# Kernel tuning notes

Hardware: AMD Instinct MI355X
Metric: run time of the kernel (lower is better)

Reference implementation:

```python
import jax, jax.numpy as jnp
import numpy as np

WS = 10
NUM_HEADS = 12
DIM = 384


def setup_inputs() -> dict:
    key = jax.random.key(0)
    k1, k2, k3 = jax.random.split(key, 3)
    B, t, H, W, C = 2, 4, 44, 44, DIM
    x = jax.random.normal(k1, (B * t, H * W, C), dtype=jnp.float32)
    qkv_w = jax.random.normal(k2, (3 * C, C), dtype=jnp.float32) * 0.02
    proj_w = jax.random.normal(k3, (C, C), dtype=jnp.float32) * 0.02
    proj_b = jnp.zeros((C,), dtype=jnp.float32)
    return {"x": x, "qkv_w": qkv_w, "proj_w": proj_w, "proj_b": proj_b,
            "t": t, "H": H, "W": W}


def reference(x, qkv_w, proj_w, proj_b, t, H, W):
    ws, nh = WS, NUM_HEADS
    BT, N, C = x.shape
    B = BT // t
    hd = C // nh
    scale = hd ** (-0.5)

    ax = x.reshape(B, t, H, W, C)
    pad_r = (ws - W % ws) % ws
    pad_b = (ws - H % ws) % ws
    if pad_r > 0 or pad_b > 0:
        ax = jnp.pad(ax, ((0, 0), (0, 0), (0, pad_b), (0, pad_r), (0, 0)))
    hg, wg = (H + ws - 1) // ws, (W + ws - 1) // ws
    # partition into windows: each window holds t*ws*ws tokens
    ax = ax.reshape(B, t, hg, ws, wg, ws, C)
    ax = ax.transpose(0, 2, 4, 1, 3, 5, 6).reshape(B, hg * wg, t * ws * ws, C)

    qkv = ax @ qkv_w.T  # (B, nw, n, 3C)
    qkv = qkv.reshape(B, hg * wg, t * ws * ws, 3, nh, hd)
    qkv = qkv.transpose(3, 0, 1, 4, 2, 5)  # (3, B, nw, nh, n, hd)
    q, k, v = qkv[0], qkv[1], qkv[2]

    attn = jnp.einsum('bwhnd,bwhmd->bwhnm', q, k) * scale
    attn = jax.nn.softmax(attn, axis=-1)
    out = jnp.einsum('bwhnm,bwhmd->bwhnd', attn, v)  # (B, nw, nh, n, hd)
    out = out.transpose(0, 1, 3, 2, 4).reshape(B, hg * wg, t * ws * ws, C)

    # reverse window partition
    out = out.reshape(B, hg, wg, t, ws, ws, C)
    out = out.transpose(0, 3, 1, 4, 2, 5, 6).reshape(B, t, hg * ws, wg * ws, C)
    out = out[:, :, :H, :W, :]
    out = out.reshape(B, t * H * W, C)
    out = out @ proj_w.T + proj_b
    return out.reshape(-1, N, C)
```

## Files before the change

kernel.cpp:

```cpp
#include <hip/hip_runtime.h>
#include <cstddef>

typedef __attribute__((ext_vector_type(8))) short bf16x8;
typedef __attribute__((ext_vector_type(4))) float f32x4;
typedef __attribute__((ext_vector_type(16))) float f32x16;
typedef unsigned short ushort_t;

namespace {
constexpr int Tt = 4, Hh = 44, Ww = 44, Cc = 384, NH = 12, HD = 32;
constexpr int NWIN = 25, NT = 400, NPOS = Hh * Ww;
constexpr int NTOK = 2 * Tt * NPOS;
constexpr float SCALE = 0.17677669529663687f;
constexpr float LOG2E = 1.4426950408889634f;
constexpr size_t XN  = (size_t)NTOK * Cc;
constexpr size_t WN  = (size_t)3 * Cc * Cc;
constexpr size_t PWN = (size_t)Cc * Cc;
constexpr size_t QKVN = (size_t)NTOK * 3 * Cc;
}

__device__ __forceinline__ ushort_t f2bf(float f) {
  unsigned u = __builtin_bit_cast(unsigned, f);
  u += 0x7fffu + ((u >> 16) & 1u);
  return (ushort_t)(u >> 16);
}

__device__ __forceinline__ unsigned cvt_pk_bf16(float a, float b) {
  unsigned r;
  asm volatile("v_cvt_pk_bf16_f32 %0, %1, %2" : "=v"(r) : "v"(a), "v"(b));
  return r;
}

__device__ __forceinline__ bf16x8 bf8zero() {
  bf16x8 v;
  v[0] = 0; v[1] = 0; v[2] = 0; v[3] = 0;
  v[4] = 0; v[5] = 0; v[6] = 0; v[7] = 0;
  return v;
}

__device__ __forceinline__ void gload16(const void* g, void* l) {
  __builtin_amdgcn_global_load_lds(
      (const __attribute__((address_space(1))) unsigned int*)g,
      (__attribute__((address_space(3))) unsigned int*)l, 16, 0, 0);
}

__device__ __forceinline__ bool win_tok(int kk, int b, int hi5, int wi5,
                                        int& tok) {
  const int tt = kk / 100, rem = kk - tt * 100;
  const int hh = rem / 10, ww2 = rem - hh * 10;
  const int h = hi5 * 10 + hh, w = wi5 * 10 + ww2;
  tok = (b * Tt + tt) * NPOS + h * Ww + w;
  return (kk < NT) && (h < Hh) && (w < Ww);
}

__global__ __launch_bounds__(256) void conv_all(
    const float* __restrict__ x, const float* __restrict__ w1,
    const float* __restrict__ w2, ushort_t* __restrict__ xo,
    ushort_t* __restrict__ w1o, ushort_t* __restrict__ w2o) {
  constexpr int XN8 = (int)(XN / 8), WN8 = (int)(WN / 8), PN8 = (int)(PWN / 8);
  int i = blockIdx.x * 256 + threadIdx.x;
  if (i >= XN8 + WN8 + PN8) return;
  const float* s;
  ushort_t* d;
  int j;
  if (i < XN8)            { s = x;  d = xo;  j = i; }
  else if (i < XN8 + WN8) { s = w1; d = w1o; j = i - XN8; }
  else                    { s = w2; d = w2o; j = i - XN8 - WN8; }
  const float4* s4 = (const float4*)s;
  float4 a = s4[2 * j], bq = s4[2 * j + 1];
  union { bf16x8 v; ushort_t u[8]; } o;
  o.u[0] = f2bf(a.x);  o.u[1] = f2bf(a.y);  o.u[2] = f2bf(a.z);  o.u[3] = f2bf(a.w);
  o.u[4] = f2bf(bq.x); o.u[5] = f2bf(bq.y); o.u[6] = f2bf(bq.z); o.u[7] = f2bf(bq.w);
  ((bf16x8*)d)[j] = o.v;
}

__global__ __launch_bounds__(256) void qkv_mfma(
    const ushort_t* __restrict__ xb, const ushort_t* __restrict__ wb,
    ushort_t* __restrict__ qkvb) {
  __shared__ __align__(16) unsigned char As[8192];
  __shared__ __align__(16) unsigned char Bs[8192];
  const int nt = blockIdx.x, mt = blockIdx.y;
  const int tid = threadIdx.x, lane = tid & 63, wid = tid >> 6;
  const int wm = wid >> 1, wn = wid & 1;
  const int g = lane >> 4, q = lane & 15;
  const int m0 = mt * 128, n0 = nt * 128;

  const unsigned char* xB = (const unsigned char*)xb;
  const unsigned char* wB = (const unsigned char*)wb;

  size_t aoff[2], boff[2];
  unsigned ldsoff[2];
#pragma unroll
  for (int p = 0; p < 2; ++p) {
    const int row = wid * 32 + p * 16 + (lane >> 2);
    const int gs = (lane & 3) ^ ((row >> 1) & 3);
    aoff[p] = (size_t)(m0 + row) * 768 + gs * 16;
    boff[p] = (size_t)(n0 + row) * 768 + gs * 16;
    ldsoff[p] = wid * 2048 + p * 1024;
  }

  f32x4 acc[4][4] = {};

  for (int kb = 0; kb < 12; ++kb) {
    if (kb) __syncthreads();
#pragma unroll
    for (int p = 0; p < 2; ++p) {
      gload16(xB + aoff[p] + kb * 64, As + ldsoff[p]);
      gload16(wB + boff[p] + kb * 64, Bs + ldsoff[p]);
    }
    __syncthreads();
    bf16x8 afr[4], bfr[4];
#pragma unroll
    for (int i = 0; i < 4; ++i) {
      const int ar = wm * 64 + i * 16 + q;
      afr[i] = *(const bf16x8*)(As + ar * 64 + ((g ^ ((ar >> 1) & 3)) << 4));
      const int br = wn * 64 + i * 16 + q;
      bfr[i] = *(const bf16x8*)(Bs + br * 64 + ((g ^ ((br >> 1) & 3)) << 4));
    }
#pragma unroll
    for (int i = 0; i < 4; ++i)
#pragma unroll
      for (int j = 0; j < 4; ++j)
        acc[i][j] = __builtin_amdgcn_mfma_f32_16x16x32_bf16(afr[i], bfr[j],
                                                            acc[i][j], 0, 0, 0);
  }

  const float QS = SCALE * LOG2E;
#pragma unroll
  for (int j = 0; j < 4; ++j) {
    const int col = n0 + wn * 64 + j * 16 + q;
    const float scl = (col < Cc) ? QS : 1.0f;
#pragma unroll
    for (int i = 0; i < 4; ++i) {
      const int rbase = m0 + wm * 64 + i * 16 + 4 * g;
#pragma unroll
      for (int r = 0; r < 4; ++r)
        qkvb[(size_t)(rbase + r) * 1152 + col] = f2bf(acc[i][j][r] * scl);
    }
  }
}

__global__ __launch_bounds__(512) void attn_mfma(
    const ushort_t* __restrict__ qkvb, ushort_t* __restrict__ aout) {
  __shared__ __align__(16) unsigned char Vt[32 * 896];

  const int blk = blockIdx.x;
  const int strip = blk & 1;
  const int wh = blk >> 1;
  const int head = wh % NH, bw = wh / NH;
  const int b = bw / NWIN, win = bw % NWIN, hi5 = win / 5, wi5 = win % 5;
  const int hoff = head * HD;

  const int tid = threadIdx.x, lane = tid & 63, wid = tid >> 6;

  for (int slot = tid; slot < 1664; slot += 512) {
    const int key = slot >> 2, dblk = (slot & 3) * 8;
    int tok;
    union { bf16x8 v; ushort_t u[8]; } t;
    if (win_tok(key, b, hi5, wi5, tok)) {
      t.v = *(const bf16x8*)(qkvb + (size_t)tok * 1152 + 768 + hoff + dblk);
    } else {
      t.v = bf8zero();
    }
    const int kc = key >> 3, klo = key & 7;
#pragma unroll
    for (int j = 0; j < 8; ++j) {
      const int d = dblk + j;
      const int f = (d & 7) ^ ((d >> 3) & 3);
      *(ushort_t*)(Vt + d * 896 + ((kc ^ f) << 4) + klo * 2) = t.u[j];
    }
  }
  __syncthreads();

  if (strip == 1 && wid >= 5) return;

  const int l31 = lane & 31, hi = lane >> 5;
  const int qrow = strip * 256 + wid * 32 + l31;
  int qtok;
  const bool qv = win_tok(qrow, b, hi5, wi5, qtok);
  const int qsrc = qv ? qtok : 0;

  const ushort_t* qp = qkvb + (size_t)qsrc * 1152 + hoff;
  const bf16x8 qf0 = *(const bf16x8*)(qp);
  const bf16x8 qf1 = *(const bf16x8*)(qp + 16);
  const bf16x8 qfa = *(const bf16x8*)(qp + hi * 8);
  const bf16x8 qfb = *(const bf16x8*)(qp + 16 + hi * 8);
  (void)qf0; (void)qf1;

  bf16x8 kf0, kf1;
  {
    int tok;
    if (win_tok(l31, b, hi5, wi5, tok)) {
      const ushort_t* kp = qkvb + (size_t)tok * 1152 + 384 + hoff;
      kf0 = *(const bf16x8*)(kp + hi * 8);
      kf1 = *(const bf16x8*)(kp + 16 + hi * 8);
    } else {
      kf0 = bf8zero();
      kf1 = bf8zero();
    }
  }

  const int fv = (l31 & 7) ^ ((l31 >> 3) & 3);
  const unsigned char* vrow = Vt + l31 * 896;

  f32x16 o = {};
  float mrun = -1e30f, lrun = 0.f;

  for (int c = 0; c < 13; ++c) {
    f32x16 s = {};
    s = __builtin_amdgcn_mfma_f32_32x32x16_bf16(kf0, qfa, s, 0, 0, 0);
    s = __builtin_amdgcn_mfma_f32_32x32x16_bf16(kf1, qfb, s, 0, 0, 0);

    if (c < 12) {
      int tok;
      if (win_tok((c + 1) * 32 + l31, b, hi5, wi5, tok)) {
        const ushort_t* kp = qkvb + (size_t)tok * 1152 + 384 + hoff;
        kf0 = *(const bf16x8*)(kp + hi * 8);
        kf1 = *(const bf16x8*)(kp + 16 + hi * 8);
      } else {
        kf0 = bf8zero();
        kf1 = bf8zero();
      }
    }

    if (c == 12) {
#pragma unroll
      for (int r = 8; r < 16; ++r) s[r] = -1e30f;
    }

    float m01 = fmaxf(s[0], s[1]),   m23 = fmaxf(s[2], s[3]);
    float m45 = fmaxf(s[4], s[5]),   m67 = fmaxf(s[6], s[7]);
    float m89 = fmaxf(s[8], s[9]),   mab = fmaxf(s[10], s[11]);
    float mcd = fmaxf(s[12], s[13]), mef = fmaxf(s[14], s[15]);
    float mc = fmaxf(fmaxf(fmaxf(m01, m23), fmaxf(m45, m67)),
                     fmaxf(fmaxf(m89, mab), fmaxf(mcd, mef)));
    mc = fmaxf(mc, __shfl_xor(mc, 32));
    const float mnew = fmaxf(mrun, mc);
    const float cf = __builtin_amdgcn_exp2f(mrun - mnew);
    mrun = mnew;

    float e[16];
#pragma unroll
    for (int r = 0; r < 16; ++r) e[r] = __builtin_amdgcn_exp2f(s[r] - mnew);
    float ps = ((e[0] + e[1]) + (e[2] + e[3])) + ((e[4] + e[5]) + (e[6] + e[7])) +
               (((e[8] + e[9]) + (e[10] + e[11])) +
                ((e[12] + e[13]) + (e[14] + e[15])));
    ps += __shfl_xor(ps, 32);
    lrun = lrun * cf + ps;
#pragma unroll
    for (int r = 0; r < 16; ++r) o[r] *= cf;

    unsigned w0 = cvt_pk_bf16(e[0], e[1]),   w1 = cvt_pk_bf16(e[2], e[3]);
    unsigned w2 = cvt_pk_bf16(e[4], e[5]),   w3 = cvt_pk_bf16(e[6], e[7]);
    unsigned w4 = cvt_pk_bf16(e[8], e[9]),   w5 = cvt_pk_bf16(e[10], e[11]);
    unsigned w6 = cvt_pk_bf16(e[12], e[13]), w7 = cvt_pk_bf16(e[14], e[15]);
    asm volatile("v_permlane32_swap_b32 %0, %1" : "+v"(w0), "+v"(w2));
    asm volatile("v_permlane32_swap_b32 %0, %1" : "+v"(w1), "+v"(w3));
    asm volatile("v_permlane32_swap_b32 %0, %1" : "+v"(w4), "+v"(w6));
    asm volatile("v_permlane32_swap_b32 %0, %1" : "+v"(w5), "+v"(w7));
    union { bf16x8 v; unsigned u[4]; } p0, p1;
    p0.u[0] = w0; p0.u[1] = w1; p0.u[2] = w2; p0.u[3] = w3;
    p1.u[0] = w4; p1.u[1] = w5; p1.u[2] = w6; p1.u[3] = w7;

    const bf16x8 vf0 = *(const bf16x8*)(vrow + (((4 * c + hi) ^ fv) << 4));
    const bf16x8 vf1 = *(const bf16x8*)(vrow + (((4 * c + 2 + hi) ^ fv) << 4));
    o = __builtin_amdgcn_mfma_f32_32x32x16_bf16(vf0, p0.v, o, 0, 0, 0);
    o = __builtin_amdgcn_mfma_f32_32x32x16_bf16(vf1, p1.v, o, 0, 0, 0);
  }

  if (qv) {
    ushort_t* dst = aout + (size_t)qtok * Cc + hoff;
    const float inv = 1.0f / lrun;
#pragma unroll
    for (int g4 = 0; g4 < 4; ++g4) {
      unsigned lo  = cvt_pk_bf16(o[4 * g4 + 0] * inv, o[4 * g4 + 1] * inv);
      unsigned hi2 = cvt_pk_bf16(o[4 * g4 + 2] * inv, o[4 * g4 + 3] * inv);
      uint2 st; st.x = lo; st.y = hi2;
      *(uint2*)(dst + 8 * g4 + 4 * hi) = st;
    }
  }
}

__global__ __launch_bounds__(256) void proj_mfma(
    const ushort_t* __restrict__ ab, const ushort_t* __restrict__ pw,
    const float* __restrict__ bias, float* __restrict__ out) {
  __shared__ __align__(16) unsigned char As[8192];
  __shared__ __align__(16) unsigned char Bs[8192];
  const int nt = blockIdx.x, mt = blockIdx.y;
  const int tid = threadIdx.x, lane = tid & 63, wid = tid >> 6;
  const int wm = wid >> 1, wn = wid & 1;
  const int g = lane >> 4, q = lane & 15;
  const int m0 = mt * 128, n0 = nt * 128;

  const unsigned char* aB = (const unsigned char*)ab;
  const unsigned char* wB = (const unsigned char*)pw;

  size_t aoff[2], boff[2];
  unsigned ldsoff[2];
#pragma unroll
  for (int p = 0; p < 2; ++p) {
    const int row = wid * 32 + p * 16 + (lane >> 2);
    const int gs = (lane & 3) ^ ((row >> 1) & 3);
    aoff[p] = (size_t)(m0 + row) * 768 + gs * 16;
    boff[p] = (size_t)(n0 + row) * 768 + gs * 16;
    ldsoff[p] = wid * 2048 + p * 1024;
  }

  f32x4 acc[4][4] = {};

  for (int kb = 0; kb < 12; ++kb) {
    if (kb) __syncthreads();
#pragma unroll
    for (int p = 0; p < 2; ++p) {
      gload16(aB + aoff[p] + kb * 64, As + ldsoff[p]);
      gload16(wB + boff[p] + kb * 64, Bs + ldsoff[p]);
    }
    __syncthreads();
    bf16x8 afr[4], bfr[4];
#pragma unroll
    for (int i = 0; i < 4; ++i) {
      const int ar = wm * 64 + i * 16 + q;
      afr[i] = *(const bf16x8*)(As + ar * 64 + ((g ^ ((ar >> 1) & 3)) << 4));
      const int br = wn * 64 + i * 16 + q;
      bfr[i] = *(const bf16x8*)(Bs + br * 64 + ((g ^ ((br >> 1) & 3)) << 4));
    }
#pragma unroll
    for (int i = 0; i < 4; ++i)
#pragma unroll
      for (int j = 0; j < 4; ++j)
        acc[i][j] = __builtin_amdgcn_mfma_f32_16x16x32_bf16(afr[i], bfr[j],
                                                            acc[i][j], 0, 0, 0);
  }

#pragma unroll
  for (int j = 0; j < 4; ++j) {
    const int col = n0 + wn * 64 + j * 16 + q;
    const float bj = bias[col];
#pragma unroll
    for (int i = 0; i < 4; ++i) {
      const int rbase = m0 + wm * 64 + i * 16 + 4 * g;
#pragma unroll
      for (int r = 0; r < 4; ++r)
        out[(size_t)(rbase + r) * Cc + col] = acc[i][j][r] + bj;
    }
  }
}

extern "C" void kernel_launch(void* const* d_in, const int* in_sizes, int n_in,
                              void* d_out, int out_size, void* d_ws,
                              size_t ws_size, hipStream_t stream) {
  const float* x      = (const float*)d_in[0];
  const float* qkv_w  = (const float*)d_in[1];
  const float* proj_w = (const float*)d_in[2];
  const float* proj_b = (const float*)d_in[3];

  ushort_t* xb    = (ushort_t*)d_ws;
  ushort_t* wb    = xb + XN;
  ushort_t* pwb   = wb + WN;
  ushort_t* qkvb  = pwb + PWN;
  ushort_t* attnb = qkvb + QKVN;

  constexpr int TOT8 = (int)((XN + WN + PWN) / 8);
  conv_all<<<(TOT8 + 255) / 256, 256, 0, stream>>>(x, qkv_w, proj_w, xb, wb, pwb);
  qkv_mfma<<<dim3(9, 121), 256, 0, stream>>>(xb, wb, qkvb);
  attn_mfma<<<1200, 512, 0, stream>>>(qkvb, attnb);
  proj_mfma<<<dim3(3, 121), 256, 0, stream>>>(attnb, pwb, proj_b, (float*)d_out);
}
```

Measured before the change: 100.00 us.

## Scatter QKV into window-major padded layout and drop online softmax max tracking

```diff
diff --git a/kernel.cpp b/kernel.cpp
--- a/kernel.cpp
+++ b/kernel.cpp
@@ -10,12 +10,13 @@
 constexpr int Tt = 4, Hh = 44, Ww = 44, Cc = 384, NH = 12, HD = 32;
 constexpr int NWIN = 25, NT = 400, NPOS = Hh * Ww;
 constexpr int NTOK = 2 * Tt * NPOS;
+constexpr int NWROW = 2 * NWIN * NT;
 constexpr float SCALE = 0.17677669529663687f;
 constexpr float LOG2E = 1.4426950408889634f;
 constexpr size_t XN  = (size_t)NTOK * Cc;
 constexpr size_t WN  = (size_t)3 * Cc * Cc;
 constexpr size_t PWN = (size_t)Cc * Cc;
-constexpr size_t QKVN = (size_t)NTOK * 3 * Cc;
+constexpr size_t QKVWN = (size_t)NWROW * 1152;
 }
 
 __device__ __forceinline__ ushort_t f2bf(float f) {
@@ -30,52 +31,56 @@
   return r;
 }
 
-__device__ __forceinline__ bf16x8 bf8zero() {
-  bf16x8 v;
-  v[0] = 0; v[1] = 0; v[2] = 0; v[3] = 0;
-  v[4] = 0; v[5] = 0; v[6] = 0; v[7] = 0;
-  return v;
-}
-
 __device__ __forceinline__ void gload16(const void* g, void* l) {
   __builtin_amdgcn_global_load_lds(
       (const __attribute__((address_space(1))) unsigned int*)g,
       (__attribute__((address_space(3))) unsigned int*)l, 16, 0, 0);
 }
 
-__device__ __forceinline__ bool win_tok(int kk, int b, int hi5, int wi5,
-                                        int& tok) {
-  const int tt = kk / 100, rem = kk - tt * 100;
-  const int hh = rem / 10, ww2 = rem - hh * 10;
-  const int h = hi5 * 10 + hh, w = wi5 * 10 + ww2;
-  tok = (b * Tt + tt) * NPOS + h * Ww + w;
-  return (kk < NT) && (h < Hh) && (w < Ww);
-}
-
 __global__ __launch_bounds__(256) void conv_all(
     const float* __restrict__ x, const float* __restrict__ w1,
     const float* __restrict__ w2, ushort_t* __restrict__ xo,
-    ushort_t* __restrict__ w1o, ushort_t* __restrict__ w2o) {
+    ushort_t* __restrict__ w1o, ushort_t* __restrict__ w2o,
+    ushort_t* __restrict__ qkvw) {
   constexpr int XN8 = (int)(XN / 8), WN8 = (int)(WN / 8), PN8 = (int)(PWN / 8);
-  int i = blockIdx.x * 256 + threadIdx.x;
-  if (i >= XN8 + WN8 + PN8) return;
-  const float* s;
-  ushort_t* d;
-  int j;
-  if (i < XN8)            { s = x;  d = xo;  j = i; }
-  else if (i < XN8 + WN8) { s = w1; d = w1o; j = i - XN8; }
-  else                    { s = w2; d = w2o; j = i - XN8 - WN8; }
-  const float4* s4 = (const float4*)s;
-  float4 a = s4[2 * j], bq = s4[2 * j + 1];
-  union { bf16x8 v; ushort_t u[8]; } o;
-  o.u[0] = f2bf(a.x);  o.u[1] = f2bf(a.y);  o.u[2] = f2bf(a.z);  o.u[3] = f2bf(a.w);
-  o.u[4] = f2bf(bq.x); o.u[5] = f2bf(bq.y); o.u[6] = f2bf(bq.z); o.u[7] = f2bf(bq.w);
-  ((bf16x8*)d)[j] = o.v;
+  constexpr int TOT8 = XN8 + WN8 + PN8;
+  constexpr int ZFN = NWROW * 9;
+  const int i = blockIdx.x * 256 + threadIdx.x;
+  if (i < TOT8) {
+    const float* s;
+    ushort_t* d;
+    int j;
+    if (i < XN8)            { s = x;  d = xo;  j = i; }
+    else if (i < XN8 + WN8) { s = w1; d = w1o; j = i - XN8; }
+    else                    { s = w2; d = w2o; j = i - XN8 - WN8; }
+    const float4* s4 = (const float4*)s;
+    float4 a = s4[2 * j], bq = s4[2 * j + 1];
+    union { bf16x8 v; ushort_t u[8]; } o;
+    o.u[0] = f2bf(a.x);  o.u[1] = f2bf(a.y);  o.u[2] = f2bf(a.z);  o.u[3] = f2bf(a.w);
+    o.u[4] = f2bf(bq.x); o.u[5] = f2bf(bq.y); o.u[6] = f2bf(bq.z); o.u[7] = f2bf(bq.w);
+    ((bf16x8*)d)[j] = o.v;
+  } else if (i < TOT8 + ZFN) {
+    const int j = i - TOT8;
+    const int row = j / 9, seg = j - row * 9;
+    const int bw = row / NT, kk = row - bw * NT;
+    const int win = bw % NWIN, hi5 = win / 5, wi5 = win % 5;
+    const int tt = kk / 100, rem = kk - tt * 100;
+    const int hh = rem / 10, ww2 = rem - hh * 10;
+    const bool invalid = (hi5 == 4 && hh >= 4) || (wi5 == 4 && ww2 >= 4);
+    (void)tt;
+    if (invalid) {
+      bf16x8* dst = (bf16x8*)(qkvw + (size_t)row * 1152 + seg * 128);
+      bf16x8 z;
+      z[0]=0;z[1]=0;z[2]=0;z[3]=0;z[4]=0;z[5]=0;z[6]=0;z[7]=0;
+#pragma unroll
+      for (int p = 0; p < 16; ++p) dst[p] = z;
+    }
+  }
 }
 
 __global__ __launch_bounds__(256) void qkv_mfma(
     const ushort_t* __restrict__ xb, const ushort_t* __restrict__ wb,
-    ushort_t* __restrict__ qkvb) {
+    ushort_t* __restrict__ qkvw) {
   __shared__ __align__(16) unsigned char As[8192];
   __shared__ __align__(16) unsigned char Bs[8192];
   const int nt = blockIdx.x, mt = blockIdx.y;
@@ -108,39 +113,47 @@
       gload16(wB + boff[p] + kb * 64, Bs + ldsoff[p]);
     }
     __syncthreads();
-    bf16x8 afr[4], bfr[4];
+    bf16x8 tfr[4], wfr[4];
 #pragma unroll
     for (int i = 0; i < 4; ++i) {
       const int ar = wm * 64 + i * 16 + q;
-      afr[i] = *(const bf16x8*)(As + ar * 64 + ((g ^ ((ar >> 1) & 3)) << 4));
+      tfr[i] = *(const bf16x8*)(As + ar * 64 + ((g ^ ((ar >> 1) & 3)) << 4));
       const int br = wn * 64 + i * 16 + q;
-      bfr[i] = *(const bf16x8*)(Bs + br * 64 + ((g ^ ((br >> 1) & 3)) << 4));
+      wfr[i] = *(const bf16x8*)(Bs + br * 64 + ((g ^ ((br >> 1) & 3)) << 4));
     }
 #pragma unroll
     for (int i = 0; i < 4; ++i)
 #pragma unroll
       for (int j = 0; j < 4; ++j)
-        acc[i][j] = __builtin_amdgcn_mfma_f32_16x16x32_bf16(afr[i], bfr[j],
+        acc[i][j] = __builtin_amdgcn_mfma_f32_16x16x32_bf16(wfr[i], tfr[j],
                                                             acc[i][j], 0, 0, 0);
   }
 
   const float QS = SCALE * LOG2E;
 #pragma unroll
   for (int j = 0; j < 4; ++j) {
-    const int col = n0 + wn * 64 + j * 16 + q;
-    const float scl = (col < Cc) ? QS : 1.0f;
+    const int t = m0 + wm * 64 + j * 16 + q;
+    const int bt = t / NPOS, pos = t - bt * NPOS;
+    const int h = pos / Ww, w = pos - h * Ww;
+    const int b = bt >> 2, tt = bt & 3;
+    const int hq = h / 10, wq = w / 10;
+    const int kk = tt * 100 + (h - hq * 10) * 10 + (w - wq * 10);
+    const int row = ((b * NWIN) + hq * 5 + wq) * NT + kk;
+    ushort_t* dst = qkvw + (size_t)row * 1152;
 #pragma unroll
     for (int i = 0; i < 4; ++i) {
-      const int rbase = m0 + wm * 64 + i * 16 + 4 * g;
-#pragma unroll
-      for (int r = 0; r < 4; ++r)
-        qkvb[(size_t)(rbase + r) * 1152 + col] = f2bf(acc[i][j][r] * scl);
+      const int col = n0 + wn * 64 + i * 16 + 4 * g;
+      const float scl = (col < Cc) ? QS : 1.0f;
+      uint2 st;
+      st.x = cvt_pk_bf16(acc[i][j][0] * scl, acc[i][j][1] * scl);
+      st.y = cvt_pk_bf16(acc[i][j][2] * scl, acc[i][j][3] * scl);
+      *(uint2*)(dst + col) = st;
     }
   }
 }
 
 __global__ __launch_bounds__(512) void attn_mfma(
-    const ushort_t* __restrict__ qkvb, ushort_t* __restrict__ aout) {
+    const ushort_t* __restrict__ qkvw, ushort_t* __restrict__ aout) {
   __shared__ __align__(16) unsigned char Vt[32 * 896];
 
   const int blk = blockIdx.x;
@@ -148,19 +161,15 @@
   const int wh = blk >> 1;
   const int head = wh % NH, bw = wh / NH;
   const int b = bw / NWIN, win = bw % NWIN, hi5 = win / 5, wi5 = win % 5;
-  const int hoff = head * HD;
 
   const int tid = threadIdx.x, lane = tid & 63, wid = tid >> 6;
+  const unsigned char* rowB = (const unsigned char*)(qkvw + (size_t)(bw * NT) * 1152);
 
   for (int slot = tid; slot < 1664; slot += 512) {
     const int key = slot >> 2, dblk = (slot & 3) * 8;
-    int tok;
+    const int kc8 = key < NT ? key : NT - 1;
     union { bf16x8 v; ushort_t u[8]; } t;
-    if (win_tok(key, b, hi5, wi5, tok)) {
-      t.v = *(const bf16x8*)(qkvb + (size_t)tok * 1152 + 768 + hoff + dblk);
-    } else {
-      t.v = bf8zero();
-    }
+    t.v = *(const bf16x8*)(rowB + (size_t)kc8 * 2304 + 1536 + head * 64 + dblk * 2);
     const int kc = key >> 3, klo = key & 7;
 #pragma unroll
     for (int j = 0; j < 8; ++j) {
@@ -175,35 +184,22 @@
 
   const int l31 = lane & 31, hi = lane >> 5;
   const int qrow = strip * 256 + wid * 32 + l31;
-  int qtok;
-  const bool qv = win_tok(qrow, b, hi5, wi5, qtok);
-  const int qsrc = qv ? qtok : 0;
-
-  const ushort_t* qp = qkvb + (size_t)qsrc * 1152 + hoff;
-  const bf16x8 qf0 = *(const bf16x8*)(qp);
-  const bf16x8 qf1 = *(const bf16x8*)(qp + 16);
-  const bf16x8 qfa = *(const bf16x8*)(qp + hi * 8);
-  const bf16x8 qfb = *(const bf16x8*)(qp + 16 + hi * 8);
-  (void)qf0; (void)qf1;
-
-  bf16x8 kf0, kf1;
-  {
-    int tok;
-    if (win_tok(l31, b, hi5, wi5, tok)) {
-      const ushort_t* kp = qkvb + (size_t)tok * 1152 + 384 + hoff;
-      kf0 = *(const bf16x8*)(kp + hi * 8);
-      kf1 = *(const bf16x8*)(kp + 16 + hi * 8);
-    } else {
-      kf0 = bf8zero();
-      kf1 = bf8zero();
-    }
-  }
+  const int qclamp = qrow < NT ? qrow : NT - 1;
+
+  const unsigned char* qp = rowB + (size_t)qclamp * 2304 + head * 64;
+  const bf16x8 qfa = *(const bf16x8*)(qp + hi * 16);
+  const bf16x8 qfb = *(const bf16x8*)(qp + 32 + hi * 16);
+
+  const unsigned char* kB = rowB + 768 + head * 64;
+  unsigned koff = (unsigned)l31 * 2304u;
+  bf16x8 kf0 = *(const bf16x8*)(kB + koff + hi * 16);
+  bf16x8 kf1 = *(const bf16x8*)(kB + koff + 32 + hi * 16);
 
   const int fv = (l31 & 7) ^ ((l31 >> 3) & 3);
   const unsigned char* vrow = Vt + l31 * 896;
 
   f32x16 o = {};
-  float mrun = -1e30f, lrun = 0.f;
+  float lpart = 0.f;
 
   for (int c = 0; c < 13; ++c) {
     f32x16 s = {};
@@ -211,15 +207,10 @@
     s = __builtin_amdgcn_mfma_f32_32x32x16_bf16(kf1, qfb, s, 0, 0, 0);
 
     if (c < 12) {
-      int tok;
-      if (win_tok((c + 1) * 32 + l31, b, hi5, wi5, tok)) {
-        const ushort_t* kp = qkvb + (size_t)tok * 1152 + 384 + hoff;
-        kf0 = *(const bf16x8*)(kp + hi * 8);
-        kf1 = *(const bf16x8*)(kp + 16 + hi * 8);
-      } else {
-        kf0 = bf8zero();
-        kf1 = bf8zero();
-      }
+      koff = (c == 11) ? (unsigned)(384 + (l31 < 16 ? l31 : 15)) * 2304u
+                       : koff + 32u * 2304u;
+      kf0 = *(const bf16x8*)(kB + koff + hi * 16);
+      kf1 = *(const bf16x8*)(kB + koff + 32 + hi * 16);
     }
 
     if (c == 12) {
@@ -227,27 +218,12 @@
       for (int r = 8; r < 16; ++r) s[r] = -1e30f;
     }
 
-    float m01 = fmaxf(s[0], s[1]),   m23 = fmaxf(s[2], s[3]);
-    float m45 = fmaxf(s[4], s[5]),   m67 = fmaxf(s[6], s[7]);
-    float m89 = fmaxf(s[8], s[9]),   mab = fmaxf(s[10], s[11]);
-    float mcd = fmaxf(s[12], s[13]), mef = fmaxf(s[14], s[15]);
-    float mc = fmaxf(fmaxf(fmaxf(m01, m23), fmaxf(m45, m67)),
-                     fmaxf(fmaxf(m89, mab), fmaxf(mcd, mef)));
-    mc = fmaxf(mc, __shfl_xor(mc, 32));
-    const float mnew = fmaxf(mrun, mc);
-    const float cf = __builtin_amdgcn_exp2f(mrun - mnew);
-    mrun = mnew;
-
     float e[16];
 #pragma unroll
-    for (int r = 0; r < 16; ++r) e[r] = __builtin_amdgcn_exp2f(s[r] - mnew);
-    float ps = ((e[0] + e[1]) + (e[2] + e[3])) + ((e[4] + e[5]) + (e[6] + e[7])) +
-               (((e[8] + e[9]) + (e[10] + e[11])) +
-                ((e[12] + e[13]) + (e[14] + e[15])));
-    ps += __shfl_xor(ps, 32);
-    lrun = lrun * cf + ps;
-#pragma unroll
-    for (int r = 0; r < 16; ++r) o[r] *= cf;
+    for (int r = 0; r < 16; ++r) e[r] = __builtin_amdgcn_exp2f(s[r]);
+    lpart += ((e[0] + e[1]) + (e[2] + e[3])) + ((e[4] + e[5]) + (e[6] + e[7])) +
+             (((e[8] + e[9]) + (e[10] + e[11])) +
+              ((e[12] + e[13]) + (e[14] + e[15])));
 
     unsigned w0 = cvt_pk_bf16(e[0], e[1]),   w1 = cvt_pk_bf16(e[2], e[3]);
     unsigned w2 = cvt_pk_bf16(e[4], e[5]),   w3 = cvt_pk_bf16(e[6], e[7]);
@@ -267,15 +243,23 @@
     o = __builtin_amdgcn_mfma_f32_32x32x16_bf16(vf1, p1.v, o, 0, 0, 0);
   }
 
-  if (qv) {
-    ushort_t* dst = aout + (size_t)qtok * Cc + hoff;
-    const float inv = 1.0f / lrun;
-#pragma unroll
-    for (int g4 = 0; g4 < 4; ++g4) {
-      unsigned lo  = cvt_pk_bf16(o[4 * g4 + 0] * inv, o[4 * g4 + 1] * inv);
-      unsigned hi2 = cvt_pk_bf16(o[4 * g4 + 2] * inv, o[4 * g4 + 3] * inv);
-      uint2 st; st.x = lo; st.y = hi2;
-      *(uint2*)(dst + 8 * g4 + 4 * hi) = st;
+  lpart += __shfl_xor(lpart, 32);
+
+  {
+    const int tt = qrow / 100, rem = qrow - tt * 100;
+    const int hh = rem / 10, ww2 = rem - hh * 10;
+    const int h = hi5 * 10 + hh, w = wi5 * 10 + ww2;
+    if (qrow < NT && h < Hh && w < Ww) {
+      const int qtok = (b * Tt + tt) * NPOS + h * Ww + w;
+      ushort_t* dst = aout + (size_t)qtok * Cc + head * HD;
+      const float inv = 1.0f / lpart;
+#pragma unroll
+      for (int g4 = 0; g4 < 4; ++g4) {
+        unsigned lo  = cvt_pk_bf16(o[4 * g4 + 0] * inv, o[4 * g4 + 1] * inv);
+        unsigned hi2 = cvt_pk_bf16(o[4 * g4 + 2] * inv, o[4 * g4 + 3] * inv);
+        uint2 st; st.x = lo; st.y = hi2;
+        *(uint2*)(dst + 8 * g4 + 4 * hi) = st;
+      }
     }
   }
 }
@@ -315,32 +299,35 @@
       gload16(wB + boff[p] + kb * 64, Bs + ldsoff[p]);
     }
     __syncthreads();
-    bf16x8 afr[4], bfr[4];
+    bf16x8 tfr[4], wfr[4];
 #pragma unroll
     for (int i = 0; i < 4; ++i) {
       const int ar = wm * 64 + i * 16 + q;
-      afr[i] = *(const bf16x8*)(As + ar * 64 + ((g ^ ((ar >> 1) & 3)) << 4));
+      tfr[i] = *(const bf16x8*)(As + ar * 64 + ((g ^ ((ar >> 1) & 3)) << 4));
       const int br = wn * 64 + i * 16 + q;
-      bfr[i] = *(const bf16x8*)(Bs + br * 64 + ((g ^ ((br >> 1) & 3)) << 4));
+      wfr[i] = *(const bf16x8*)(Bs + br * 64 + ((g ^ ((br >> 1) & 3)) << 4));
     }
 #pragma unroll
     for (int i = 0; i < 4; ++i)
 #pragma unroll
       for (int j = 0; j < 4; ++j)
-        acc[i][j] = __builtin_amdgcn_mfma_f32_16x16x32_bf16(afr[i], bfr[j],
+        acc[i][j] = __builtin_amdgcn_mfma_f32_16x16x32_bf16(wfr[i], tfr[j],
                                                             acc[i][j], 0, 0, 0);
   }
 
 #pragma unroll
   for (int j = 0; j < 4; ++j) {
-    const int col = n0 + wn * 64 + j * 16 + q;
-    const float bj = bias[col];
+    const int t = m0 + wm * 64 + j * 16 + q;
 #pragma unroll
     for (int i = 0; i < 4; ++i) {
-      const int rbase = m0 + wm * 64 + i * 16 + 4 * g;
-#pragma unroll
-      for (int r = 0; r < 4; ++r)
-        out[(size_t)(rbase + r) * Cc + col] = acc[i][j][r] + bj;
+      const int col = n0 + wn * 64 + i * 16 + 4 * g;
+      const float4 bb = *(const float4*)(bias + col);
+      float4 st;
+      st.x = acc[i][j][0] + bb.x;
+      st.y = acc[i][j][1] + bb.y;
+      st.z = acc[i][j][2] + bb.z;
+      st.w = acc[i][j][3] + bb.w;
+      *(float4*)(out + (size_t)t * Cc + col) = st;
     }
   }
 }
@@ -356,12 +343,14 @@
   ushort_t* xb    = (ushort_t*)d_ws;
   ushort_t* wb    = xb + XN;
   ushort_t* pwb   = wb + WN;
-  ushort_t* qkvb  = pwb + PWN;
-  ushort_t* attnb = qkvb + QKVN;
+  ushort_t* qkvw  = pwb + PWN;
+  ushort_t* attnb = qkvw + QKVWN;
 
   constexpr int TOT8 = (int)((XN + WN + PWN) / 8);
-  conv_all<<<(TOT8 + 255) / 256, 256, 0, stream>>>(x, qkv_w, proj_w, xb, wb, pwb);
-  qkv_mfma<<<dim3(9, 121), 256, 0, stream>>>(xb, wb, qkvb);
-  attn_mfma<<<1200, 512, 0, stream>>>(qkvb, attnb);
+  constexpr int ZFN = NWROW * 9;
+  conv_all<<<(TOT8 + ZFN + 255) / 256, 256, 0, stream>>>(x, qkv_w, proj_w, xb,
+                                                         wb, pwb, qkvw);
+  qkv_mfma<<<dim3(9, 121), 256, 0, stream>>>(xb, wb, qkvw);
+  attn_mfma<<<1200, 512, 0, stream>>>(qkvw, attnb);
   proj_mfma<<<dim3(3, 121), 256, 0, stream>>>(attnb, pwb, proj_b, (float*)d_out);
 }
```

New measurement: 116.0 us. 1.16x slower.
